# Kernel optimization log

Measured on AMD Instinct MI355X. Metric: run time of the kernel, lower is better.

## Reference

```python
import jax, jax.numpy as jnp
import numpy as np
from jax import lax

NUM_CLASSES = 21
KSIZE = 11
DIL = 1
BLUR = 4
NUM_STEPS = 5
YX_SCALE = 80.0
RGB_SCALE = 13.0
POS_SCALE = 3.0


def _ceil_pad_factor(sizes, factor):
    offs = tuple((factor - s % factor) % factor for s in sizes)
    return tuple((o + 1) // 2 for o in offs)


def avg_pool_nopad(x, k, pad):
    # F.avg_pool2d(kernel=stride=k, padding=pad, count_include_pad=False)
    pcfg = ((0, 0), (0, 0), (pad[0], pad[0]), (pad[1], pad[1]))
    s = lax.reduce_window(x, jnp.float32(0), lax.add, (1, 1, k, k), (1, 1, k, k), pcfg)
    ones = jnp.ones((1, 1) + x.shape[2:], x.dtype)
    cnt = lax.reduce_window(ones, jnp.float32(0), lax.add, (1, 1, k, k), (1, 1, k, k), pcfg)
    return s / cnt


def _patches(x, k, dil):
    # im2col with zero padding (matches torch F.unfold used by pac)
    pad = (k // 2) * dil
    p = lax.conv_general_dilated_patches(
        x, (k, k), (1, 1), [(pad, pad), (pad, pad)], rhs_dilation=(dil, dil))
    B, C, H, W = x.shape
    return p.reshape(B, C, k * k, H, W)


def gaussian_kernel(feat, k, dil):
    # pixel-adaptive Gaussian kernel: exp(-0.5 * ||f_i - f_j||^2) over the KxK window
    p = _patches(feat, k, dil)                       # [B,F,k2,H,W]
    d = p - feat[:, :, None]
    return jnp.exp(-0.5 * jnp.sum(d * d, axis=1))    # [B,k2,H,W]


def pac_message(Q, kernel, k, dil):
    # shared-filter (Potts, spatial_filter=False) pac conv: per-channel kernel-weighted sum
    p = _patches(Q, k, dil)                          # [B,C,k2,h,w]
    return jnp.einsum('bckhw,bkhw->bchw', p, kernel)


def upsample_bilinear(x, scale):
    # matches F.interpolate(mode='bilinear', align_corners=False)
    B, C, h, w = x.shape
    def idx_w(n_in):
        n_out = n_in * scale
        src = jnp.clip((jnp.arange(n_out, dtype=jnp.float32) + 0.5) / scale - 0.5, 0.0, n_in - 1.0)
        i0 = jnp.floor(src).astype(jnp.int32)
        i1 = jnp.minimum(i0 + 1, n_in - 1)
        return i0, i1, (src - i0).astype(x.dtype)
    y0, y1, wy = idx_w(h)
    x0, x1, wx = idx_w(w)
    xh = x[:, :, y0, :] * (1 - wy)[None, None, :, None] + x[:, :, y1, :] * wy[None, None, :, None]
    return xh[:, :, :, x0] * (1 - wx)[None, None, None, :] + xh[:, :, :, x1] * wx[None, None, None, :]


def crf_forward(x, w_backbone, b_backbone, unary_weight, pairwise_weights):
    B, _, H, W = x.shape
    # backbone stub: 3x3 conv producing unary logits [B,21,H,W]
    unary = lax.conv_general_dilated(
        x, w_backbone, (1, 1), [(1, 1), (1, 1)],
        dimension_numbers=('NCHW', 'OIHW', 'NCHW')) + b_backbone[None, :, None, None]
    # edge features: bilateral (YX/80, RGB/13) and spatial (YX/3)
    yx = jnp.stack(jnp.meshgrid(jnp.arange(H, dtype=x.dtype), jnp.arange(W, dtype=x.dtype), indexing='ij'))
    yx = jnp.broadcast_to(yx[None], (B, 2, H, W))
    feat_bilateral = jnp.concatenate([yx / YX_SCALE, x / RGB_SCALE], axis=1)  # [B,5,H,W]
    feat_spatial = yx / POS_SCALE                                             # [B,2,H,W]
    pad = _ceil_pad_factor((H, W), BLUR)
    kernels = [gaussian_kernel(avg_pool_nopad(f, BLUR, pad), KSIZE, DIL)
               for f in (feat_bilateral, feat_spatial)]

    def step(logQ, unary, k1, k2, uw, pw):
        Q = jax.nn.softmax(logQ, axis=1)
        Qb = avg_pool_nopad(Q, BLUR, pad)
        new = uw * unary
        for kern, w in ((k1, pw[0]), (k2, pw[1])):
            msg = pac_message(Qb, kern, KSIZE, DIL)
            msg = upsample_bilinear(msg, BLUR)[:, :, pad[0]:pad[0] + H, pad[1]:pad[1] + W]
            new = new + w * msg
        return new

    logQ = unary
    for _ in range(NUM_STEPS):
        logQ = step(logQ, unary, kernels[0], kernels[1], unary_weight, pairwise_weights)
    return logQ  # final_output == 'log_Q'


def setup_inputs():
    key = jax.random.key(0)
    ks = jax.random.split(key, 3)
    B, H, W = 2, 512, 512
    x = jax.random.uniform(ks[0], (B, 3, H, W), jnp.float32) * 255.0  # image in [0,255]
    w_backbone = jax.random.normal(ks[1], (NUM_CLASSES, 3, 3, 3), jnp.float32) * 0.1
    b_backbone = jax.random.normal(ks[2], (NUM_CLASSES,), jnp.float32) * 0.01
    unary_weight = jnp.asarray(0.8, jnp.float32)
    pairwise_weights = jnp.asarray([2.0, 0.6], jnp.float32)
    return {"x": x, "w_backbone": w_backbone, "b_backbone": b_backbone,
            "unary_weight": unary_weight, "pairwise_weights": pairwise_weights}


def reference(x, w_backbone, b_backbone, unary_weight, pairwise_weights):
    return crf_forward(x, w_backbone, b_backbone, unary_weight, pairwise_weights)
```

## Files before the change

kernel.cpp:

```cpp
#include <hip/hip_runtime.h>

#define NCH 21
#define HWP (1 << 14)
#define KS 11
#define KK 121
#define PTW 32
#define PTH 8
#define LROW 48
#define LHGT 18
#define LPLANE (LROW * LHGT)

typedef _Float16 half4 __attribute__((ext_vector_type(4)));

__global__ __launch_bounds__(256) void k_conv_sm(const float* __restrict__ x,
                                                 const float* __restrict__ w,
                                                 const float* __restrict__ bias,
                                                 float* __restrict__ unary,
                                                 float* __restrict__ qb) {
    int idx = blockIdx.x * 256 + threadIdx.x;
    int r = idx & 3;
    int xqi = (idx >> 2) & 127;
    int py = (idx >> 9) & 127;
    int b = idx >> 16;
    int y = 4 * py + r;
    int xq = xqi << 2;

    float p[3][3][6];
#pragma unroll
    for (int ch = 0; ch < 3; ++ch) {
        const float* xp = x + (((size_t)(b * 3 + ch)) << 18);
#pragma unroll
        for (int rr = 0; rr < 3; ++rr) {
            int yy = y + rr - 1;
            if ((unsigned)yy >= 512u) {
#pragma unroll
                for (int j = 0; j < 6; ++j) p[ch][rr][j] = 0.f;
            } else {
                const float* row = xp + (yy << 9);
                float4 v = *(const float4*)(row + xq);
                p[ch][rr][1] = v.x; p[ch][rr][2] = v.y; p[ch][rr][3] = v.z; p[ch][rr][4] = v.w;
                p[ch][rr][0] = (xq > 0) ? row[xq - 1] : 0.f;
                p[ch][rr][5] = (xq + 4 < 512) ? row[xq + 4] : 0.f;
            }
        }
    }
    float a[NCH][4];
    for (int o = 0; o < NCH; ++o) {
        const float* wp = w + o * 27;
        float bz = bias[o];
        float a0 = bz, a1 = bz, a2 = bz, a3 = bz;
#pragma unroll
        for (int ch = 0; ch < 3; ++ch)
#pragma unroll
            for (int rr = 0; rr < 3; ++rr) {
                float w0 = wp[ch * 9 + rr * 3 + 0];
                float w1 = wp[ch * 9 + rr * 3 + 1];
                float w2 = wp[ch * 9 + rr * 3 + 2];
                const float* pr = p[ch][rr];
                a0 += w0 * pr[0] + w1 * pr[1] + w2 * pr[2];
                a1 += w0 * pr[1] + w1 * pr[2] + w2 * pr[3];
                a2 += w0 * pr[2] + w1 * pr[3] + w2 * pr[4];
                a3 += w0 * pr[3] + w1 * pr[4] + w2 * pr[5];
            }
        *(float4*)(unary + (((size_t)(b * NCH + o)) << 18) + (y << 9) + xq) =
            make_float4(a0, a1, a2, a3);
        a[o][0] = a0; a[o][1] = a1; a[o][2] = a2; a[o][3] = a3;
    }
    float qsum[NCH];
#pragma unroll
    for (int c = 0; c < NCH; ++c) qsum[c] = 0.f;
#pragma unroll
    for (int i2 = 0; i2 < 4; ++i2) {
        float m = a[0][i2];
#pragma unroll
        for (int c = 1; c < NCH; ++c) m = fmaxf(m, a[c][i2]);
        float s = 0.f;
#pragma unroll
        for (int c = 0; c < NCH; ++c) { float e = __expf(a[c][i2] - m); a[c][i2] = e; s += e; }
        float inv = 1.0f / s;
#pragma unroll
        for (int c = 0; c < NCH; ++c) qsum[c] += a[c][i2] * inv;
    }
#pragma unroll
    for (int c = 0; c < NCH; ++c) {
        float v = qsum[c];
        v += __shfl_xor(v, 1);
        v += __shfl_xor(v, 2);
        if (r == 0) qb[(((size_t)(b * NCH + c)) << 14) + (py << 7) + xqi] = v * 0.0625f;
    }
}

__global__ __launch_bounds__(256) void k_pool_rgb(const float* __restrict__ x,
                                                  float* __restrict__ prgb) {
    int idx = blockIdx.x * 256 + threadIdx.x;
    int p = idx & (HWP - 1);
    int ch = (idx >> 14) % 3;
    int b = idx / (3 * HWP);
    int py = p >> 7, px = p & 127;
    const float* xp = x + (((size_t)(b * 3 + ch)) << 18);
    float s = 0.f;
#pragma unroll
    for (int r = 0; r < 4; ++r) {
        const float4 v = *(const float4*)(xp + (((4 * py + r) << 9) + 4 * px));
        s += v.x + v.y + v.z + v.w;
    }
    prgb[idx] = s * 0.0625f;
}

__global__ __launch_bounds__(256) void k_build_kc(const float* __restrict__ prgb,
                                                  const float* __restrict__ pw,
                                                  _Float16* __restrict__ kc) {
    int idx = blockIdx.x * 256 + threadIdx.x;
    int p = idx & (HWP - 1);
    int jj = idx >> 14;
    int b = (jj >= KK) ? 1 : 0;
    int j = jj - KK * b;
    int dy = j / KS, dx = j - dy * KS;
    int py = p >> 7, px = p & 127;
    float pw0 = pw[0], pw1 = pw[1];

    const float inv13 = 1.0f / 13.0f;
    float fy = (4.f * py + 1.5f) * (1.0f / 80.0f);
    float fx = (4.f * px + 1.5f) * (1.0f / 80.0f);
    const float* pb = prgb + (size_t)b * 3 * HWP;
    float r0 = pb[p] * inv13;
    float g0 = pb[HWP + p] * inv13;
    float b0 = pb[2 * HWP + p] * inv13;
    float sy = (4.f * py + 1.5f) * (1.0f / 3.0f);
    float sx = (4.f * px + 1.5f) * (1.0f / 3.0f);

    int ny = py + dy - 5;
    int nx = px + dx - 5;
    float s1, s2;
    if ((unsigned)ny < 128u && (unsigned)nx < 128u) {
        int np = (ny << 7) + nx;
        float r2 = pb[np] * inv13;
        float g2 = pb[HWP + np] * inv13;
        float b2 = pb[2 * HWP + np] * inv13;
        float dya = fy - (4.f * ny + 1.5f) * (1.0f / 80.0f);
        float dxa = fx - (4.f * nx + 1.5f) * (1.0f / 80.0f);
        float dr = r0 - r2, dg = g0 - g2, db = b0 - b2;
        s1 = dya * dya + dxa * dxa + dr * dr + dg * dg + db * db;
        float dys = sy - (4.f * ny + 1.5f) * (1.0f / 3.0f);
        float dxs = sx - (4.f * nx + 1.5f) * (1.0f / 3.0f);
        s2 = dys * dys + dxs * dxs;
    } else {
        s1 = fy * fy + fx * fx + r0 * r0 + g0 * g0 + b0 * b0;
        s2 = sy * sy + sx * sx;
    }
    kc[idx] = (_Float16)(pw0 * __expf(-0.5f * s1) + pw1 * __expf(-0.5f * s2));
}

__global__ __launch_bounds__(256) void k_pac4(const float* __restrict__ qb,
                                              const _Float16* __restrict__ kc,
                                              float* __restrict__ msgc) {
    int tile = blockIdx.x & 63;
    int cg = (blockIdx.x >> 6) % 6;
    int b = blockIdx.x / 384;
    int tx0 = (tile & 3) * PTW;
    int ty0 = (tile >> 2) * PTH;
    int c0 = cg * 4;

    __shared__ float lq[4 * LPLANE];

    const float* qbb = qb + (((size_t)(b * NCH)) << 14);
    for (int i = threadIdx.x; i < 4 * LPLANE; i += 256) {
        int c = i / LPLANE;
        int rem = i - c * LPLANE;
        int ly = rem / LROW;
        int lx = rem - ly * LROW;
        int ch = c0 + c;
        int gy = ty0 + ly - 5, gx = tx0 + lx - 5;
        float v = 0.f;
        if (ch < NCH && lx < 42 && (unsigned)gy < 128u && (unsigned)gx < 128u)
            v = qbb[((size_t)ch << 14) + (gy << 7) + gx];
        lq[i] = v;
    }
    __syncthreads();

    int s = threadIdx.x & 63;
    int cl = threadIdx.x >> 6;
    int my = s >> 3;
    int mx0 = (s & 7) << 2;
    int ch = c0 + cl;

    float acc0 = 0.f, acc1 = 0.f, acc2 = 0.f, acc3 = 0.f;
    int p0 = ((ty0 + my) << 7) + tx0 + mx0;
    const _Float16* kcb = kc + (((size_t)(b * KK)) << 14) + p0;
    const float* lbase = lq + cl * LPLANE + mx0;

    for (int dy = 0; dy < KS; ++dy) {
        const float* lp = lbase + (my + dy) * LROW;
        float4 v0 = *(const float4*)(lp + 0);
        float4 v1 = *(const float4*)(lp + 4);
        float4 v2 = *(const float4*)(lp + 8);
        float4 v3 = *(const float4*)(lp + 12);
        float rb[16] = {v0.x, v0.y, v0.z, v0.w, v1.x, v1.y, v1.z, v1.w,
                        v2.x, v2.y, v2.z, v2.w, v3.x, v3.y, v3.z, v3.w};
        const _Float16* kcrow = kcb + (((size_t)(dy * KS)) << 14);
#pragma unroll
        for (int dx = 0; dx < KS; ++dx) {
            half4 k4 = *(const half4*)(kcrow + (((size_t)dx) << 14));
            acc0 += (float)k4.x * rb[dx + 0];
            acc1 += (float)k4.y * rb[dx + 1];
            acc2 += (float)k4.z * rb[dx + 2];
            acc3 += (float)k4.w * rb[dx + 3];
        }
    }
    if (ch < NCH)
        *(float4*)(msgc + (((size_t)(b * NCH + ch)) << 14) + p0) =
            make_float4(acc0, acc1, acc2, acc3);
}

__global__ __launch_bounds__(256) void k_step(const float* __restrict__ unary,
                                              const float* __restrict__ msgc,
                                              const float* __restrict__ uwp,
                                              float* __restrict__ qb,
                                              float* __restrict__ out,
                                              int write_out) {
    int half = blockIdx.x & 1;
    int py = (blockIdx.x >> 1) & 127;
    int b = blockIdx.x >> 8;
    int px0 = half << 6;

    __shared__ float lmsg[NCH * 3 * 66];

    const float* mbase = msgc + (((size_t)(b * NCH)) << 14);
    for (int i = threadIdx.x; i < NCH * 198; i += 256) {
        int c = i / 198;
        int rem = i - c * 198;
        int row = rem / 66;
        int j = rem - row * 66;
        int ry = min(max(py - 1 + row, 0), 127);
        int gx = min(max(px0 - 1 + j, 0), 127);
        lmsg[i] = mbase[((size_t)c << 14) + (ry << 7) + gx];
    }
    __syncthreads();

    int r = threadIdx.x & 3;
    int lpx = threadIdx.x >> 2;
    int px = px0 + lpx;
    int y = 4 * py + r;
    float uw = uwp[0];

    int iA = (r < 2) ? 0 : 1;
    int iB = iA + 1;
    float fy = (r == 0) ? 0.625f : (r == 1) ? 0.875f : (r == 2) ? 0.125f : 0.375f;

    size_t base = (((size_t)(b * NCH)) << 18) + (y << 9) + (px << 2);
    const float* up = unary + base;

    float a[NCH][4];
#pragma unroll
    for (int c = 0; c < NCH; ++c) {
        float4 u4 = *(const float4*)(up + ((size_t)c << 18));
        const float* lA = lmsg + c * 198 + iA * 66 + lpx;
        const float* lB = lmsg + c * 198 + iB * 66 + lpx;
        float aL = lA[0], aM = lA[1], aR = lA[2];
        float bL = lB[0], bM = lB[1], bR = lB[2];
        float cL = aL + (bL - aL) * fy;
        float cM = aM + (bM - aM) * fy;
        float cR = aR + (bR - aR) * fy;
        a[c][0] = uw * u4.x + cL + (cM - cL) * 0.625f;
        a[c][1] = uw * u4.y + cL + (cM - cL) * 0.875f;
        a[c][2] = uw * u4.z + cM + (cR - cM) * 0.125f;
        a[c][3] = uw * u4.w + cM + (cR - cM) * 0.375f;
    }

    if (write_out) {
        float* op = out + base;
#pragma unroll
        for (int c = 0; c < NCH; ++c)
            *(float4*)(op + ((size_t)c << 18)) = make_float4(a[c][0], a[c][1], a[c][2], a[c][3]);
        return;
    }

    float qsum[NCH];
#pragma unroll
    for (int c = 0; c < NCH; ++c) qsum[c] = 0.f;
#pragma unroll
    for (int i2 = 0; i2 < 4; ++i2) {
        float m = a[0][i2];
#pragma unroll
        for (int c = 1; c < NCH; ++c) m = fmaxf(m, a[c][i2]);
        float ss = 0.f;
#pragma unroll
        for (int c = 0; c < NCH; ++c) { float e = __expf(a[c][i2] - m); a[c][i2] = e; ss += e; }
        float inv = 1.0f / ss;
#pragma unroll
        for (int c = 0; c < NCH; ++c) qsum[c] += a[c][i2] * inv;
    }
#pragma unroll
    for (int c = 0; c < NCH; ++c) {
        float v = qsum[c];
        v += __shfl_xor(v, 1);
        v += __shfl_xor(v, 2);
        if (r == 0) qb[(((size_t)(b * NCH + c)) << 14) + (py << 7) + px] = v * 0.0625f;
    }
}

extern "C" void kernel_launch(void* const* d_in, const int* in_sizes, int n_in,
                              void* d_out, int out_size, void* d_ws, size_t ws_size,
                              hipStream_t stream) {
    const float* x  = (const float*)d_in[0];
    const float* wb = (const float*)d_in[1];
    const float* bb = (const float*)d_in[2];
    const float* uw = (const float*)d_in[3];
    const float* pw = (const float*)d_in[4];
    float* out = (float*)d_out;

    float* ws    = (float*)d_ws;
    float* unary = ws;
    _Float16* kc = (_Float16*)(unary + 11010048);
    float* qb    = (float*)(kc + 3964928);
    float* msgc  = qb + 688128;
    float* prgb  = msgc;

    k_conv_sm<<<512, 256, 0, stream>>>(x, wb, bb, unary, qb);
    k_pool_rgb<<<384, 256, 0, stream>>>(x, prgb);
    k_build_kc<<<15488, 256, 0, stream>>>(prgb, pw, kc);

    for (int s = 0; s < 5; ++s) {
        k_pac4<<<768, 256, 0, stream>>>(qb, kc, msgc);
        k_step<<<512, 256, 0, stream>>>(unary, msgc, uw, qb, out, (s == 4) ? 1 : 0);
    }
}
```

Measured before the change: 272.9 us.

## Store unary in pixel-major padded layout and assign one pixel per thread in step

The unary buffer moves from a channel-planar layout to a pixel-major layout with a 24-float stride, so each thread in k_step reads its 21 channels as contiguous vector loads. k_step is remapped so each thread handles one full-resolution pixel instead of four. The grid grows to 2048 blocks, each with a smaller shared-memory tile, and the softmax pooling is reduced across 16 lanes with shuffles. The intent is to cut register pressure and raise occupancy in k_step. The cost is strided, uncoalesced 4-byte stores of unary in the conv kernel, scalar rather than float4 stores of the final output, and a larger workspace.

Result: slower. 303.2 us (+11.1%).

```diff
diff --git a/kernel.cpp b/kernel.cpp
--- a/kernel.cpp
+++ b/kernel.cpp
@@ -4,6 +4,7 @@
 #define HWP (1 << 14)
 #define KS 11
 #define KK 121
+#define USTR 24
 #define PTW 32
 #define PTH 8
 #define LROW 48
@@ -62,9 +63,14 @@
                 a2 += w0 * pr[2] + w1 * pr[3] + w2 * pr[4];
                 a3 += w0 * pr[3] + w1 * pr[4] + w2 * pr[5];
             }
-        *(float4*)(unary + (((size_t)(b * NCH + o)) << 18) + (y << 9) + xq) =
-            make_float4(a0, a1, a2, a3);
         a[o][0] = a0; a[o][1] = a1; a[o][2] = a2; a[o][3] = a3;
+    }
+    size_t pixbase = (((size_t)b) << 18) + (y << 9) + xq;
+#pragma unroll
+    for (int i = 0; i < 4; ++i) {
+        float* up = unary + (pixbase + i) * USTR;
+#pragma unroll
+        for (int o = 0; o < NCH; ++o) up[o] = a[o][i];
     }
     float qsum[NCH];
 #pragma unroll
@@ -218,84 +224,85 @@
                                               float* __restrict__ qb,
                                               float* __restrict__ out,
                                               int write_out) {
-    int half = blockIdx.x & 1;
-    int py = (blockIdx.x >> 1) & 127;
-    int b = blockIdx.x >> 8;
-    int px0 = half << 6;
-
-    __shared__ float lmsg[NCH * 3 * 66];
+    int px0 = (blockIdx.x & 7) << 4;
+    int py = (blockIdx.x >> 3) & 127;
+    int b = blockIdx.x >> 10;
+
+    __shared__ float lmsg[NCH * 54];
 
     const float* mbase = msgc + (((size_t)(b * NCH)) << 14);
-    for (int i = threadIdx.x; i < NCH * 198; i += 256) {
-        int c = i / 198;
-        int rem = i - c * 198;
-        int row = rem / 66;
-        int j = rem - row * 66;
+    for (int i = threadIdx.x; i < NCH * 54; i += 256) {
+        int c = i / 54;
+        int rem = i - c * 54;
+        int row = rem / 18;
+        int j = rem - row * 18;
         int ry = min(max(py - 1 + row, 0), 127);
         int gx = min(max(px0 - 1 + j, 0), 127);
         lmsg[i] = mbase[((size_t)c << 14) + (ry << 7) + gx];
     }
     __syncthreads();
 
-    int r = threadIdx.x & 3;
-    int lpx = threadIdx.x >> 2;
-    int px = px0 + lpx;
+    int sub = threadIdx.x & 15;
+    int lp = threadIdx.x >> 4;
+    int r = sub >> 2, i2 = sub & 3;
+    int px = px0 + lp;
     int y = 4 * py + r;
+    int x = 4 * px + i2;
     float uw = uwp[0];
 
     int iA = (r < 2) ? 0 : 1;
-    int iB = iA + 1;
     float fy = (r == 0) ? 0.625f : (r == 1) ? 0.875f : (r == 2) ? 0.125f : 0.375f;
-
-    size_t base = (((size_t)(b * NCH)) << 18) + (y << 9) + (px << 2);
-    const float* up = unary + base;
-
-    float a[NCH][4];
+    int jA = (i2 < 2) ? lp : lp + 1;
+    float fx = (i2 == 0) ? 0.625f : (i2 == 1) ? 0.875f : (i2 == 2) ? 0.125f : 0.375f;
+    int oA = iA * 18 + jA, oB = oA + 18;
+
+    const float* up = unary + ((((size_t)b) << 18) + (y << 9) + x) * USTR;
+    float4 u0 = *(const float4*)(up);
+    float4 u1 = *(const float4*)(up + 4);
+    float4 u2 = *(const float4*)(up + 8);
+    float4 u3 = *(const float4*)(up + 12);
+    float4 u4 = *(const float4*)(up + 16);
+    float u20 = up[20];
+
+    float v[NCH];
 #pragma unroll
     for (int c = 0; c < NCH; ++c) {
-        float4 u4 = *(const float4*)(up + ((size_t)c << 18));
-        const float* lA = lmsg + c * 198 + iA * 66 + lpx;
-        const float* lB = lmsg + c * 198 + iB * 66 + lpx;
-        float aL = lA[0], aM = lA[1], aR = lA[2];
-        float bL = lB[0], bM = lB[1], bR = lB[2];
-        float cL = aL + (bL - aL) * fy;
-        float cM = aM + (bM - aM) * fy;
-        float cR = aR + (bR - aR) * fy;
-        a[c][0] = uw * u4.x + cL + (cM - cL) * 0.625f;
-        a[c][1] = uw * u4.y + cL + (cM - cL) * 0.875f;
-        a[c][2] = uw * u4.z + cM + (cR - cM) * 0.125f;
-        a[c][3] = uw * u4.w + cM + (cR - cM) * 0.375f;
-    }
+        const float* lc = lmsg + c * 54;
+        float m00 = lc[oA], m01 = lc[oA + 1];
+        float m10 = lc[oB], m11 = lc[oB + 1];
+        float vA = m00 + (m10 - m00) * fy;
+        float vB = m01 + (m11 - m01) * fy;
+        v[c] = vA + (vB - vA) * fx;
+    }
+    v[0] += uw * u0.x;  v[1] += uw * u0.y;  v[2] += uw * u0.z;  v[3] += uw * u0.w;
+    v[4] += uw * u1.x;  v[5] += uw * u1.y;  v[6] += uw * u1.z;  v[7] += uw * u1.w;
+    v[8] += uw * u2.x;  v[9] += uw * u2.y;  v[10] += uw * u2.z; v[11] += uw * u2.w;
+    v[12] += uw * u3.x; v[13] += uw * u3.y; v[14] += uw * u3.z; v[15] += uw * u3.w;
+    v[16] += uw * u4.x; v[17] += uw * u4.y; v[18] += uw * u4.z; v[19] += uw * u4.w;
+    v[20] += uw * u20;
 
     if (write_out) {
-        float* op = out + base;
-#pragma unroll
-        for (int c = 0; c < NCH; ++c)
-            *(float4*)(op + ((size_t)c << 18)) = make_float4(a[c][0], a[c][1], a[c][2], a[c][3]);
+        float* op = out + (((size_t)(b * NCH)) << 18) + (y << 9) + x;
+#pragma unroll
+        for (int c = 0; c < NCH; ++c) op[(size_t)c << 18] = v[c];
         return;
     }
 
-    float qsum[NCH];
-#pragma unroll
-    for (int c = 0; c < NCH; ++c) qsum[c] = 0.f;
-#pragma unroll
-    for (int i2 = 0; i2 < 4; ++i2) {
-        float m = a[0][i2];
-#pragma unroll
-        for (int c = 1; c < NCH; ++c) m = fmaxf(m, a[c][i2]);
-        float ss = 0.f;
-#pragma unroll
-        for (int c = 0; c < NCH; ++c) { float e = __expf(a[c][i2] - m); a[c][i2] = e; ss += e; }
-        float inv = 1.0f / ss;
-#pragma unroll
-        for (int c = 0; c < NCH; ++c) qsum[c] += a[c][i2] * inv;
-    }
+    float m = v[0];
+#pragma unroll
+    for (int c = 1; c < NCH; ++c) m = fmaxf(m, v[c]);
+    float ss = 0.f;
+#pragma unroll
+    for (int c = 0; c < NCH; ++c) { v[c] = __expf(v[c] - m); ss += v[c]; }
+    float inv = 1.0f / ss;
 #pragma unroll
     for (int c = 0; c < NCH; ++c) {
-        float v = qsum[c];
-        v += __shfl_xor(v, 1);
-        v += __shfl_xor(v, 2);
-        if (r == 0) qb[(((size_t)(b * NCH + c)) << 14) + (py << 7) + px] = v * 0.0625f;
+        float q = v[c] * inv;
+        q += __shfl_xor(q, 1, 16);
+        q += __shfl_xor(q, 2, 16);
+        q += __shfl_xor(q, 4, 16);
+        q += __shfl_xor(q, 8, 16);
+        if (sub == 0) qb[(((size_t)(b * NCH + c)) << 14) + (py << 7) + px] = q * 0.0625f;
     }
 }
 
@@ -311,7 +318,7 @@
 
     float* ws    = (float*)d_ws;
     float* unary = ws;
-    _Float16* kc = (_Float16*)(unary + 11010048);
+    _Float16* kc = (_Float16*)(unary + 12582912);
     float* qb    = (float*)(kc + 3964928);
     float* msgc  = qb + 688128;
     float* prgb  = msgc;
@@ -322,6 +329,6 @@
 
     for (int s = 0; s < 5; ++s) {
         k_pac4<<<768, 256, 0, stream>>>(qb, kc, msgc);
-        k_step<<<512, 256, 0, stream>>>(unary, msgc, uw, qb, out, (s == 4) ? 1 : 0);
-    }
-}
+        k_step<<<2048, 256, 0, stream>>>(unary, msgc, uw, qb, out, (s == 4) ? 1 : 0);
+    }
+}
```
